# Kernel tuning notes

Hardware: AMD Instinct MI355X
Metric: run time of the kernel (lower is better)

The kernel has to match this reference:

```python
import jax, jax.numpy as jnp
import numpy as np

NUM_HEADS = 8  # attention_head_size = C // NUM_HEADS, used only for score scaling


def conv1x1(x, w, b):
    # x: [B, Cin, H, W], w: [Cout, Cin], b: [Cout]
    return jnp.einsum('bchw,oc->bohw', x, w) + b[None, :, None, None]


def setup_inputs() -> dict:
    key = jax.random.key(0)
    ks = jax.random.split(key, 10)
    B, C, H, W = 8, 256, 96, 96
    x = jax.random.normal(ks[0], (B, C, H, W), dtype=jnp.float32)
    y = jax.random.normal(ks[1], (B, 1, 24, 24), dtype=jnp.float32)
    s = 0.02
    wy = jax.random.normal(ks[2], (C, 1), dtype=jnp.float32) * s
    by = jnp.zeros((C,), dtype=jnp.float32)
    wq = jax.random.normal(ks[3], (C, C), dtype=jnp.float32) * s
    bq = jnp.zeros((C,), dtype=jnp.float32)
    wk = jax.random.normal(ks[4], (C, C), dtype=jnp.float32) * s
    bk = jnp.zeros((C,), dtype=jnp.float32)
    wv = jax.random.normal(ks[5], (C, C), dtype=jnp.float32) * s
    bv = jnp.zeros((C,), dtype=jnp.float32)
    return {'x': x, 'y': y, 'wy': wy, 'by': by, 'wq': wq, 'bq': bq,
            'wk': wk, 'bk': bk, 'wv': wv, 'bv': bv}


def reference(x, y, wy, by, wq, bq, wk, bk, wv, bv):
    B, C, H, W = x.shape
    head_size = C // NUM_HEADS
    # x branch
    xq = conv1x1(x, wq, bq)
    xk = conv1x1(x, wk, bk)
    v = conv1x1(x, wv, bv)
    # y branch: 1 -> C channels, bilinear upsample (align_corners=False == half-pixel)
    y2 = conv1x1(y, wy, by)
    y2 = jax.image.resize(y2, (B, C, H, W), method='bilinear')
    yq = conv1x1(y2, wq, bq)
    yk = conv1x1(y2, wk, bk)
    # gated Q/K
    q = (xq * yq).transpose(0, 2, 1, 3)  # [B, H, C, W]
    k = (xk * yk).transpose(0, 2, 1, 3)
    vt = v.transpose(0, 2, 1, 3)
    # channel attention per spatial row: scores [B, H, C, C]
    scores = jnp.einsum('bhcw,bhdw->bhcd', q, k) / jnp.sqrt(jnp.asarray(head_size, x.dtype))
    probs = jax.nn.softmax(scores, axis=-1)
    out = jnp.einsum('bhcd,bhdw->bhcw', probs, vt)
    return out.transpose(0, 2, 1, 3)  # [B, C, H, W]
```

## Files before the change

### kernel.cpp

```cpp
#include <hip/hip_runtime.h>

typedef __bf16 bf16;
typedef __attribute__((ext_vector_type(8))) __bf16 bf16x8;
typedef __attribute__((ext_vector_type(4))) __bf16 bf16x4;
typedef __attribute__((ext_vector_type(4))) float f32x4;

#define MFMA16(A, B, C) __builtin_amdgcn_mfma_f32_16x16x32_bf16(A, B, C, 0, 0, 0)

static __device__ __forceinline__ void wave_lgkm_wait() {
  asm volatile("s_waitcnt lgkmcnt(0)" ::: "memory");
}

__global__ __launch_bounds__(256) void k_prep(
    const float* __restrict__ y, const float* __restrict__ wy, const float* __restrict__ by,
    const float* __restrict__ wq, const float* __restrict__ bq,
    const float* __restrict__ wk, const float* __restrict__ bk,
    const float* __restrict__ wv,
    bf16* __restrict__ wq_bf, bf16* __restrict__ wk_bf, bf16* __restrict__ wv_bf,
    float* __restrict__ yu, float* __restrict__ aq, float* __restrict__ cq,
    float* __restrict__ ak, float* __restrict__ ck)
{
  int blk = blockIdx.x, t = threadIdx.x;
  if (blk < 192) {
    int idx4 = blk * 256 + t;
    int fo = idx4 * 4;
    const float* src; bf16* dst; int off;
    if (fo < 65536)       { src = wq; dst = wq_bf; off = fo; }
    else if (fo < 131072) { src = wk; dst = wk_bf; off = fo - 65536; }
    else                  { src = wv; dst = wv_bf; off = fo - 131072; }
    float4 v = *(const float4*)(src + off);
    bf16x4 o;
    o[0] = (bf16)v.x; o[1] = (bf16)v.y; o[2] = (bf16)v.z; o[3] = (bf16)v.w;
    *(bf16x4*)(dst + off) = o;
  } else if (blk < 200) {
    int b = blk - 192;
    const float* yb = y + b * 576;
#pragma unroll 1
    for (int i = 0; i < 36; ++i) {
      int e = t + i * 256;
      int oh = e / 96, ow = e % 96;
      float sh = oh * 0.25f - 0.375f;
      float sw = ow * 0.25f - 0.375f;
      int ih0 = (int)floorf(sh);
      int iw0 = (int)floorf(sw);
      float fh = sh - (float)ih0, fw = sw - (float)iw0;
      int ih0c = min(23, max(0, ih0)), ih1c = min(23, max(0, ih0 + 1));
      int iw0c = min(23, max(0, iw0)), iw1c = min(23, max(0, iw0 + 1));
      float v00 = yb[ih0c * 24 + iw0c], v01 = yb[ih0c * 24 + iw1c];
      float v10 = yb[ih1c * 24 + iw0c], v11 = yb[ih1c * 24 + iw1c];
      yu[b * 9216 + e] = (1.0f - fh) * ((1.0f - fw) * v00 + fw * v01)
                       + fh * ((1.0f - fw) * v10 + fw * v11);
    }
  } else {
    int ol = t >> 5, cl = t & 31;
    int o = (blk - 200) * 8 + ol;
    int c0 = cl * 8;
    float4 wy0 = *(const float4*)(wy + c0), wy1 = *(const float4*)(wy + c0 + 4);
    float4 by0 = *(const float4*)(by + c0), by1 = *(const float4*)(by + c0 + 4);
    float4 q0  = *(const float4*)(wq + o * 256 + c0), q1 = *(const float4*)(wq + o * 256 + c0 + 4);
    float4 k0  = *(const float4*)(wk + o * 256 + c0), k1 = *(const float4*)(wk + o * 256 + c0 + 4);
    float wyv[8] = {wy0.x, wy0.y, wy0.z, wy0.w, wy1.x, wy1.y, wy1.z, wy1.w};
    float byv[8] = {by0.x, by0.y, by0.z, by0.w, by1.x, by1.y, by1.z, by1.w};
    float qv[8]  = {q0.x, q0.y, q0.z, q0.w, q1.x, q1.y, q1.z, q1.w};
    float kv[8]  = {k0.x, k0.y, k0.z, k0.w, k1.x, k1.y, k1.z, k1.w};
    float saq = 0.f, scq = 0.f, sak = 0.f, sck = 0.f;
#pragma unroll
    for (int j = 0; j < 8; ++j) {
      saq += qv[j] * wyv[j]; scq += qv[j] * byv[j];
      sak += kv[j] * wyv[j]; sck += kv[j] * byv[j];
    }
#pragma unroll
    for (int s = 16; s >= 1; s >>= 1) {
      saq += __shfl_xor(saq, s, 32);
      scq += __shfl_xor(scq, s, 32);
      sak += __shfl_xor(sak, s, 32);
      sck += __shfl_xor(sck, s, 32);
    }
    if (cl == 0) {
      aq[o] = saq; cq[o] = scq + bq[o];
      ak[o] = sak; ck[o] = sck + bk[o];
    }
  }
}

__global__ __launch_bounds__(1024, 1) void k_fused(
    const float* __restrict__ x, const float* __restrict__ yu,
    const bf16* __restrict__ wq_bf, const bf16* __restrict__ wk_bf, const bf16* __restrict__ wv_bf,
    const float* __restrict__ bq, const float* __restrict__ bk, const float* __restrict__ bv,
    const float* __restrict__ aq, const float* __restrict__ cq,
    const float* __restrict__ ak, const float* __restrict__ ck,
    float* __restrict__ out)
{
  __shared__ __align__(16) bf16 xs[96 * 264];
  __shared__ __align__(16) bf16 ks[256 * 104];
  __shared__ __align__(16) bf16 bounce[2][16 * 16 * 40];

  int pl = blockIdx.x;
  int b = pl / 96, h = pl % 96;
  int t = threadIdx.x;
  int wid = t >> 6, lane = t & 63;
  int l15 = lane & 15, g = lane >> 4;
  int otile = wid * 16;

  {
    const float* xrow = x + (size_t)b * 2359296 + (size_t)h * 96;
#pragma unroll
    for (int i = 0; i < 3; ++i) {
      int tsk = i * 1024 + t;
      int w = tsk % 96;
      int c0 = (tsk / 96) * 8;
      float v[8];
#pragma unroll
      for (int j = 0; j < 8; ++j) v[j] = xrow[(size_t)(c0 + j) * 9216 + w];
      bf16x8 o8;
#pragma unroll
      for (int j = 0; j < 8; ++j) o8[j] = (bf16)v[j];
      *(bf16x8*)(xs + w * 264 + c0) = o8;
    }
  }
  __syncthreads();

  const float SC = 0.17677669529663687f;
  bf16* stg = ks + otile * 104;

  bf16x8 qf[3];

  {
    f32x4 qacc[6] = {};
    f32x4 kacc[6] = {};
    f32x4 vacc[6] = {};
#pragma unroll 1
    for (int kq = 0; kq < 8; ++kq) {
      const bf16* xp = xs + kq * 32 + g * 8;
      bf16x8 A[6];
#pragma unroll
      for (int m = 0; m < 6; ++m)
        A[m] = *(const bf16x8*)(xp + (m * 16 + l15) * 264);
      size_t wo = (size_t)(otile + l15) * 256 + kq * 32 + g * 8;
      bf16x8 Bq = *(const bf16x8*)(wq_bf + wo);
      bf16x8 Bk = *(const bf16x8*)(wk_bf + wo);
      bf16x8 Bv = *(const bf16x8*)(wv_bf + wo);
#pragma unroll
      for (int m = 0; m < 6; ++m) {
        qacc[m] = MFMA16(A[m], Bq, qacc[m]);
        kacc[m] = MFMA16(A[m], Bk, kacc[m]);
        vacc[m] = MFMA16(Bv, A[m], vacc[m]);
      }
    }

    float4 yv[6];
    {
      const float* yr = yu + (size_t)pl * 96;
#pragma unroll
      for (int mt = 0; mt < 6; ++mt)
        yv[mt] = *(const float4*)(yr + mt * 16 + g * 4);
    }
    int o = otile + l15;
    float bqv = bq[o], aq0 = aq[o], cq0 = cq[o];
    float bkv = bk[o], ak0 = ak[o], ck0 = ck[o];

#pragma unroll
    for (int m = 0; m < 6; ++m) {
      float yy[4] = {yv[m].x, yv[m].y, yv[m].z, yv[m].w};
      bf16x4 pk;
#pragma unroll
      for (int r = 0; r < 4; ++r)
        pk[r] = (bf16)((qacc[m][r] + bqv) * (yy[r] * aq0 + cq0) * SC);
      *(bf16x4*)(stg + l15 * 104 + m * 16 + g * 4) = pk;
    }
    wave_lgkm_wait();
#pragma unroll
    for (int kk = 0; kk < 3; ++kk)
      qf[kk] = *(const bf16x8*)(stg + l15 * 104 + kk * 32 + g * 8);
    wave_lgkm_wait();

#pragma unroll
    for (int m = 0; m < 6; ++m) {
      float yy[4] = {yv[m].x, yv[m].y, yv[m].z, yv[m].w};
      bf16x4 pk;
#pragma unroll
      for (int r = 0; r < 4; ++r)
        pk[r] = (bf16)((kacc[m][r] + bkv) * (yy[r] * ak0 + ck0));
      *(bf16x4*)(ks + (size_t)o * 104 + m * 16 + g * 4) = pk;
    }

    float4 bm = *(const float4*)(bv + otile + g * 4);
    float bb[4] = {bm.x, bm.y, bm.z, bm.w};
    __syncthreads();
    bf16* vs = xs;
#pragma unroll
    for (int n = 0; n < 6; ++n) {
      bf16x4 pk;
#pragma unroll
      for (int r = 0; r < 4; ++r) pk[r] = (bf16)(vacc[n][r] + bb[r]);
      *(bf16x4*)(vs + (size_t)(n * 16 + l15) * 264 + otile + g * 4) = pk;
    }
  }
  __syncthreads();

  const bf16* vs = xs;
  f32x4 oacc[6] = {};
  float lp[4] = {0.f, 0.f, 0.f, 0.f};

#pragma unroll 1
  for (int dt = 0; dt < 8; ++dt) {
    int d0 = dt * 32;
    f32x4 s[2] = {};
    const bf16* kp = ks + (size_t)(d0 + l15) * 104 + g * 8;
    __builtin_amdgcn_s_setprio(1);
#pragma unroll
    for (int kk = 0; kk < 3; ++kk) {
#pragma unroll
      for (int dn = 0; dn < 2; ++dn) {
        bf16x8 B = *(const bf16x8*)(kp + (size_t)dn * 16 * 104 + kk * 32);
        s[dn] = MFMA16(qf[kk], B, s[dn]);
      }
    }
    __builtin_amdgcn_s_setprio(0);
    bf16* bnc = bounce[dt & 1] + wid * (16 * 40);
#pragma unroll
    for (int dn = 0; dn < 2; ++dn) {
#pragma unroll
      for (int r = 0; r < 4; ++r) {
        float e = __expf(s[dn][r]);
        lp[r] += e;
        bnc[(g * 4 + r) * 40 + dn * 16 + l15] = (bf16)e;
      }
    }
    wave_lgkm_wait();
    bf16x8 pa = *(const bf16x8*)(bnc + l15 * 40 + g * 8);
    const bf16* vp = vs + (size_t)l15 * 264 + d0 + g * 8;
    __builtin_amdgcn_s_setprio(1);
#pragma unroll
    for (int n = 0; n < 6; ++n) {
      bf16x8 Bv = *(const bf16x8*)(vp + (size_t)n * 16 * 264);
      oacc[n] = MFMA16(pa, Bv, oacc[n]);
    }
    __builtin_amdgcn_s_setprio(0);
  }

  float inv[4];
#pragma unroll
  for (int r = 0; r < 4; ++r) {
    float v = lp[r];
    v += __shfl_xor(v, 1, 16);
    v += __shfl_xor(v, 2, 16);
    v += __shfl_xor(v, 4, 16);
    v += __shfl_xor(v, 8, 16);
    inv[r] = 1.0f / v;
  }

  __syncthreads();
  float* fst = (float*)ks;
  int s_hi = wid >> 3;
  int lr = (wid & 7) * 16;
  float* ob = out + (size_t)b * 2359296 + (size_t)h * 96;
#pragma unroll 1
  for (int s = 0; s < 2; ++s) {
    if (s_hi == s) {
#pragma unroll
      for (int n = 0; n < 6; ++n)
#pragma unroll
        for (int r = 0; r < 4; ++r)
          fst[(lr + g * 4 + r) * 100 + n * 16 + l15] = oacc[n][r] * inv[r];
    }
    __syncthreads();
    int ob0 = s * 128;
#pragma unroll
    for (int it = 0; it < 3; ++it) {
      int idx = it * 1024 + t;
      int row = idx / 24, col = idx - row * 24;
      float4 v4 = *(const float4*)(fst + row * 100 + col * 4);
      *(float4*)(ob + (size_t)(ob0 + row) * 9216 + col * 4) = v4;
    }
    __syncthreads();
  }
}

extern "C" void kernel_launch(void* const* d_in, const int* in_sizes, int n_in,
                              void* d_out, int out_size, void* d_ws, size_t ws_size,
                              hipStream_t stream) {
  const float* x  = (const float*)d_in[0];
  const float* y  = (const float*)d_in[1];
  const float* wy = (const float*)d_in[2];
  const float* by = (const float*)d_in[3];
  const float* wq = (const float*)d_in[4];
  const float* bq = (const float*)d_in[5];
  const float* wk = (const float*)d_in[6];
  const float* bk = (const float*)d_in[7];
  const float* wv = (const float*)d_in[8];
  const float* bv = (const float*)d_in[9];
  float* out = (float*)d_out;

  char* wsb = (char*)d_ws;
  bf16* wq_bf = (bf16*)(wsb);
  bf16* wk_bf = (bf16*)(wsb + 131072);
  bf16* wv_bf = (bf16*)(wsb + 262144);
  float* yu   = (float*)(wsb + 393216);
  float* aq   = (float*)(wsb + 688128);
  float* cq   = (float*)(wsb + 689152);
  float* ak   = (float*)(wsb + 690176);
  float* ck   = (float*)(wsb + 691200);

  hipLaunchKernelGGL(k_prep, dim3(232), dim3(256), 0, stream,
                     y, wy, by, wq, bq, wk, bk, wv,
                     wq_bf, wk_bf, wv_bf, yu, aq, cq, ak, ck);
  hipLaunchKernelGGL(k_fused, dim3(768), dim3(1024), 0, stream,
                     x, yu, wq_bf, wk_bf, wv_bf, bq, bk, bv,
                     aq, cq, ak, ck, out);
}
```

Before: 223.1 us.

## Compute transposed scores to keep softmax probs in registers, prefetch K fragments

```diff
diff --git a/kernel.cpp b/kernel.cpp
--- a/kernel.cpp
+++ b/kernel.cpp
@@ -93,7 +93,6 @@
 {
   __shared__ __align__(16) bf16 xs[96 * 264];
   __shared__ __align__(16) bf16 ks[256 * 104];
-  __shared__ __align__(16) bf16 bounce[2][16 * 16 * 40];
 
   int pl = blockIdx.x;
   int b = pl / 96, h = pl % 96;
@@ -188,47 +187,58 @@
     float bb[4] = {bm.x, bm.y, bm.z, bm.w};
     __syncthreads();
     bf16* vs = xs;
+    int vbase = (otile & ~16) + ((otile >> 2) & 4);
 #pragma unroll
     for (int n = 0; n < 6; ++n) {
       bf16x4 pk;
 #pragma unroll
       for (int r = 0; r < 4; ++r) pk[r] = (bf16)(vacc[n][r] + bb[r]);
-      *(bf16x4*)(vs + (size_t)(n * 16 + l15) * 264 + otile + g * 4) = pk;
+      *(bf16x4*)(vs + (size_t)(n * 16 + l15) * 264 + vbase + g * 8) = pk;
     }
   }
   __syncthreads();
 
   const bf16* vs = xs;
   f32x4 oacc[6] = {};
-  float lp[4] = {0.f, 0.f, 0.f, 0.f};
-
-#pragma unroll 1
-  for (int dt = 0; dt < 8; ++dt) {
+  float lp = 0.f;
+
+  bf16x8 KA[6], KB[6];
+  {
+    const bf16* kp = ks + (size_t)l15 * 104 + g * 8;
+#pragma unroll
+    for (int kk = 0; kk < 3; ++kk)
+#pragma unroll
+      for (int dn = 0; dn < 2; ++dn)
+        KA[kk * 2 + dn] = *(const bf16x8*)(kp + (size_t)(dn * 16) * 104 + kk * 32);
+  }
+
+  auto attn_step = [&](int dt, bf16x8* Kc, bf16x8* Kn, bool pf) {
     int d0 = dt * 32;
-    f32x4 s[2] = {};
-    const bf16* kp = ks + (size_t)(d0 + l15) * 104 + g * 8;
+    if (pf) {
+      const bf16* kp = ks + (size_t)((dt + 1) * 32 + l15) * 104 + g * 8;
+#pragma unroll
+      for (int kk = 0; kk < 3; ++kk)
+#pragma unroll
+        for (int dn = 0; dn < 2; ++dn)
+          Kn[kk * 2 + dn] = *(const bf16x8*)(kp + (size_t)(dn * 16) * 104 + kk * 32);
+    }
+    f32x4 s0 = {}, s1 = {};
     __builtin_amdgcn_s_setprio(1);
 #pragma unroll
     for (int kk = 0; kk < 3; ++kk) {
-#pragma unroll
-      for (int dn = 0; dn < 2; ++dn) {
-        bf16x8 B = *(const bf16x8*)(kp + (size_t)dn * 16 * 104 + kk * 32);
-        s[dn] = MFMA16(qf[kk], B, s[dn]);
-      }
+      s0 = MFMA16(Kc[kk * 2 + 0], qf[kk], s0);
+      s1 = MFMA16(Kc[kk * 2 + 1], qf[kk], s1);
     }
     __builtin_amdgcn_s_setprio(0);
-    bf16* bnc = bounce[dt & 1] + wid * (16 * 40);
-#pragma unroll
-    for (int dn = 0; dn < 2; ++dn) {
-#pragma unroll
-      for (int r = 0; r < 4; ++r) {
-        float e = __expf(s[dn][r]);
-        lp[r] += e;
-        bnc[(g * 4 + r) * 40 + dn * 16 + l15] = (bf16)e;
-      }
-    }
-    wave_lgkm_wait();
-    bf16x8 pa = *(const bf16x8*)(bnc + l15 * 40 + g * 8);
+    bf16x8 pa;
+#pragma unroll
+    for (int r = 0; r < 4; ++r) {
+      float e0 = __expf(s0[r]);
+      float e1 = __expf(s1[r]);
+      lp += e0 + e1;
+      pa[r] = (bf16)e0;
+      pa[4 + r] = (bf16)e1;
+    }
     const bf16* vp = vs + (size_t)l15 * 264 + d0 + g * 8;
     __builtin_amdgcn_s_setprio(1);
 #pragma unroll
@@ -237,18 +247,22 @@
       oacc[n] = MFMA16(pa, Bv, oacc[n]);
     }
     __builtin_amdgcn_s_setprio(0);
-  }
-
-  float inv[4];
-#pragma unroll
-  for (int r = 0; r < 4; ++r) {
-    float v = lp[r];
-    v += __shfl_xor(v, 1, 16);
-    v += __shfl_xor(v, 2, 16);
-    v += __shfl_xor(v, 4, 16);
-    v += __shfl_xor(v, 8, 16);
-    inv[r] = 1.0f / v;
-  }
+  };
+
+#pragma unroll 1
+  for (int dt2 = 0; dt2 < 4; ++dt2) {
+    attn_step(2 * dt2,     KA, KB, true);
+    attn_step(2 * dt2 + 1, KB, KA, 2 * dt2 + 1 < 7);
+  }
+
+  float vsum = lp;
+  vsum += __shfl_xor(vsum, 16, 64);
+  vsum += __shfl_xor(vsum, 32, 64);
+  float inv = 1.0f / vsum;
+  float invr[4];
+#pragma unroll
+  for (int r = 0; r < 4; ++r)
+    invr[r] = __shfl(inv, g * 4 + r, 16);
 
   __syncthreads();
   float* fst = (float*)ks;
@@ -262,7 +276,7 @@
       for (int n = 0; n < 6; ++n)
 #pragma unroll
         for (int r = 0; r < 4; ++r)
-          fst[(lr + g * 4 + r) * 100 + n * 16 + l15] = oacc[n][r] * inv[r];
+          fst[(lr + g * 4 + r) * 100 + n * 16 + l15] = oacc[n][r] * invr[r];
     }
     __syncthreads();
     int ob0 = s * 128;
```

New measurement: 216.1 us. 3.1% less time.
